# Optimization experiments

Hardware: AMD Instinct MI355X
Metric: run time of the kernel (lower is better)

The kernel has to match this reference:

```python
import jax, jax.numpy as jnp
import numpy as np

INC, ICS = 32, 8      # in_caps, in_caps_size
ONC, OCS = 32, 16     # out_caps, out_caps_size
K, STRIDE, PAD = 3, 1, 0
ITERS = 3


def squash(t, axis=-1):
    sq = jnp.sum(t * t, axis=axis, keepdims=True)
    return (sq / (1.0 + sq)) * t / jnp.sqrt(sq)


def setup_inputs() -> dict:
    key = jax.random.key(0)
    k1, k2 = jax.random.split(key)
    x = jax.random.normal(k1, (4, INC * ICS, 14, 14), dtype=jnp.float32)
    # nn.Parameter(torch.randn(...)); scaled by 1/sqrt(ICS) for numerical sanity
    weight = jax.random.normal(k2, (ONC, INC * K * K, ICS, OCS), dtype=jnp.float32) * (1.0 / np.sqrt(ICS))
    return {"x": x, "weight": weight}


def reference(x, weight):
    B, C, H, W = x.shape
    OH = (H + 2 * PAD - K) // STRIDE + 1
    OW = (W + 2 * PAD - K) // STRIDE + 1
    # Tile2d: extract KxK patches -> (B, C*K*K, OH, OW), channel order (C, kh, kw)
    patches = jax.lax.conv_general_dilated_patches(
        x, (K, K), (STRIDE, STRIDE), padding=((PAD, PAD), (PAD, PAD)))
    # (B, INC, ICS, K*K, OH*OW) -> (B, OH*OW, K*K, INC, ICS) -> (N, KK*INC, ICS)
    tiles = patches.reshape(B, INC, ICS, K * K, OH * OW)
    tiles = tiles.transpose(0, 4, 3, 1, 2).reshape(B * OH * OW, K * K * INC, ICS)

    # priors: (ONC, N, KKI, OCS)  == x[None,:,:,None,:] @ W[:,None]
    priors = jnp.einsum('nki,okic->onkc', tiles, weight)

    # dynamic routing; logits broadcast over OCS in the original (identical math)
    N = B * OH * OW
    KKI = K * K * INC
    logits = jnp.zeros((ONC, N, KKI, 1), dtype=priors.dtype)
    outputs = None
    for i in range(ITERS):
        probs = jax.nn.softmax(logits, axis=2)              # over KKI routes
        outputs = squash(jnp.sum(probs * priors, axis=2, keepdims=True))  # (ONC,N,1,OCS)
        if i != ITERS - 1:
            logits = logits + jnp.sum(priors * outputs, axis=-1, keepdims=True)

    # (ONC, N, OCS) -> (N, ONC, OCS) -> (B, ONC*OCS, OH, OW)
    out = outputs[:, :, 0, :].transpose(1, 0, 2)
    out = out.reshape(B, OH, OW, ONC * OCS).transpose(0, 3, 1, 2)
    return out
```

## Files before the change

kernel.cpp:

```cpp
#include <hip/hip_runtime.h>

static constexpr int OHW = 12, NSP = 144;

__global__ void build_T(const float* __restrict__ x, float4* __restrict__ T4) {
    const int g = blockIdx.x * 256 + threadIdx.x;
    const int n = g / 576;
    const int q = g - n * 576;
    const int r = q << 2;
    const int k = r >> 3;
    const int i0 = r & 7;
    const int ic = k & 31;
    const int kk = k >> 5;
    const int kh = kk / 3, kw = kk - kh * 3;
    const int b = n / NSP;
    const int rm = n - b * NSP;
    const int oh = rm / OHW, ow = rm - oh * OHW;
    const float* xp = x + (size_t)(b * 256 + ic * 8 + i0) * 196
                        + (oh + kh) * 14 + (ow + kw);
    float4 v;
    v.x = xp[0];
    v.y = xp[196];
    v.z = xp[392];
    v.w = xp[588];
    T4[g] = v;
}

__device__ __forceinline__ void fma4(float4& a, float s, const float4& w) {
    a.x = fmaf(s, w.x, a.x);
    a.y = fmaf(s, w.y, a.y);
    a.z = fmaf(s, w.z, a.z);
    a.w = fmaf(s, w.w, a.w);
}

__device__ __forceinline__ float4 shfl_xor4(const float4& v, int m) {
    float4 r;
    r.x = __shfl_xor(v.x, m);
    r.y = __shfl_xor(v.y, m);
    r.z = __shfl_xor(v.z, m);
    r.w = __shfl_xor(v.w, m);
    return r;
}

__device__ __forceinline__ void do_j(const float4* __restrict__ T4,
                                     const float4* __restrict__ W4,
                                     float4* __restrict__ Pl,
                                     int o, int nbase, int k, int cg,
                                     int g_local, int lane) {
    float4 w[8];
    const float4* wp = W4 + (size_t)(o * 288 + k) * 32 + cg;
    #pragma unroll
    for (int i = 0; i < 8; ++i) w[i] = wp[i * 4];
    #pragma unroll
    for (int nn = 0; nn < 4; ++nn) {
        const float4* tp = T4 + (size_t)(nbase + nn) * 576 + k * 2;
        const float4 t0 = tp[0];
        const float4 t1 = tp[1];
        float4 a = make_float4(0.f, 0.f, 0.f, 0.f);
        fma4(a, t0.x, w[0]); fma4(a, t0.y, w[1]);
        fma4(a, t0.z, w[2]); fma4(a, t0.w, w[3]);
        fma4(a, t1.x, w[4]); fma4(a, t1.y, w[5]);
        fma4(a, t1.z, w[6]); fma4(a, t1.w, w[7]);
        Pl[nn * 576 + g_local * 64 + lane] = a;
    }
}

__global__ __launch_bounds__(256, 4)
void caps_main(const float4* __restrict__ T4, const float4* __restrict__ W4,
               float* __restrict__ out) {
    __shared__ float4 Pl[4 * 9 * 64];
    const int tid = threadIdx.x;
    const int o = blockIdx.y;
    const int nbase = blockIdx.x * 4;
    const int cg = tid & 3;
    const int kg = tid >> 2;
    const int wv = tid >> 6;
    const int lane = tid & 63;

    float4 P[18];

    #pragma unroll
    for (int j = 0; j < 5; ++j) {
        const int k = kg + 64 * j;
        const int g = wv + 4 * j;
        if (k < 288 && g < 9)
            do_j(T4, W4, Pl, o, nbase, k, cg, g, lane);
    }
    __syncthreads();
    #pragma unroll
    for (int jj = 0; jj < 9; ++jj)
        P[jj] = Pl[wv * 576 + jj * 64 + lane];
    __syncthreads();
    #pragma unroll
    for (int j = 0; j < 5; ++j) {
        const int k = kg + 64 * j;
        const int g = wv + 4 * j;
        if (k < 288 && g >= 9)
            do_j(T4, W4, Pl, o, nbase, k, cg, g - 9, lane);
    }
    __syncthreads();
    #pragma unroll
    for (int jj = 9; jj < 18; ++jj)
        P[jj] = Pl[wv * 576 + (jj - 9) * 64 + lane];

    float lj[18];
    #pragma unroll
    for (int jj = 0; jj < 18; ++jj) lj[jj] = 0.f;
    float4 vq = make_float4(0.f, 0.f, 0.f, 0.f);

    #pragma unroll
    for (int it = 0; it < 3; ++it) {
        float4 svU = make_float4(0.f, 0.f, 0.f, 0.f);
        float S;
        if (it == 0) {
            #pragma unroll
            for (int jj = 0; jj < 18; ++jj) {
                svU.x += P[jj].x; svU.y += P[jj].y;
                svU.z += P[jj].z; svU.w += P[jj].w;
            }
            #pragma unroll
            for (int m = 4; m < 64; m <<= 1) {
                const float4 t = shfl_xor4(svU, m);
                svU.x += t.x; svU.y += t.y; svU.z += t.z; svU.w += t.w;
            }
            S = 288.0f;
        } else {
            S = 0.f;
            #pragma unroll
            for (int jj = 0; jj < 18; ++jj) {
                const float e = __expf(lj[jj]);
                S += e;
                fma4(svU, e, P[jj]);
            }
            #pragma unroll
            for (int m = 4; m < 64; m <<= 1) {
                const float4 t = shfl_xor4(svU, m);
                svU.x += t.x; svU.y += t.y; svU.z += t.z; svU.w += t.w;
                S += __shfl_xor(S, m);
            }
        }
        const float invS = __frcp_rn(S);
        float4 s;
        s.x = svU.x * invS; s.y = svU.y * invS;
        s.z = svU.z * invS; s.w = svU.w * invS;
        float sq = s.x * s.x + s.y * s.y + s.z * s.z + s.w * s.w;
        sq += __shfl_xor(sq, 1);
        sq += __shfl_xor(sq, 2);
        const float scale = __fsqrt_rn(sq) / (1.0f + sq);
        vq.x = s.x * scale; vq.y = s.y * scale;
        vq.z = s.z * scale; vq.w = s.w * scale;

        if (it < 2) {
            #pragma unroll
            for (int jj = 0; jj < 18; ++jj) {
                float d = P[jj].x * vq.x + P[jj].y * vq.y +
                          P[jj].z * vq.z + P[jj].w * vq.w;
                d += __shfl_xor(d, 1);
                d += __shfl_xor(d, 2);
                lj[jj] += d;
            }
        }
    }

    if ((lane >> 2) == 0) {
        const int n = nbase + wv;
        const int b = n / NSP;
        const int rm = n - b * NSP;
        float* op = out + (size_t)(b * 512 + o * 16 + cg * 4) * NSP + rm;
        op[0 * NSP] = vq.x;
        op[1 * NSP] = vq.y;
        op[2 * NSP] = vq.z;
        op[3 * NSP] = vq.w;
    }
}

extern "C" void kernel_launch(void* const* d_in, const int* in_sizes, int n_in,
                              void* d_out, int out_size, void* d_ws, size_t ws_size,
                              hipStream_t stream) {
    const float* x  = (const float*)d_in[0];
    const float* wt = (const float*)d_in[1];
    float* out = (float*)d_out;
    float4* T4 = (float4*)d_ws;

    build_T<<<dim3(576 * 576 / 256), 256, 0, stream>>>(x, T4);
    caps_main<<<dim3(144, 32), 256, 0, stream>>>(T4, (const float4*)wt, out);
}
```

Baseline: 125.4 us.

## Fuse patch extraction into capsule kernel using shared-memory input tiles

Removes the separate im2col kernel and its global workspace. Each block now loads a 3x8 spatial window of all 256 input channels into LDS with a swizzled layout, builds priors for 6 output positions directly from LDS, and routes them. The block grows to 384 threads (6 positions) in a 96x32 grid. This saves one launch and the T4 write/read traffic, at the cost of more LDS per block and occupancy changes.

Result: slower. 154.9 us (+23.5%).

```diff
diff --git a/kernel.cpp b/kernel.cpp
--- a/kernel.cpp
+++ b/kernel.cpp
@@ -1,29 +1,6 @@
 #include <hip/hip_runtime.h>
 
-static constexpr int OHW = 12, NSP = 144;
-
-__global__ void build_T(const float* __restrict__ x, float4* __restrict__ T4) {
-    const int g = blockIdx.x * 256 + threadIdx.x;
-    const int n = g / 576;
-    const int q = g - n * 576;
-    const int r = q << 2;
-    const int k = r >> 3;
-    const int i0 = r & 7;
-    const int ic = k & 31;
-    const int kk = k >> 5;
-    const int kh = kk / 3, kw = kk - kh * 3;
-    const int b = n / NSP;
-    const int rm = n - b * NSP;
-    const int oh = rm / OHW, ow = rm - oh * OHW;
-    const float* xp = x + (size_t)(b * 256 + ic * 8 + i0) * 196
-                        + (oh + kh) * 14 + (ow + kw);
-    float4 v;
-    v.x = xp[0];
-    v.y = xp[196];
-    v.z = xp[392];
-    v.w = xp[588];
-    T4[g] = v;
-}
+static constexpr int NSP = 144;
 
 __device__ __forceinline__ void fma4(float4& a, float s, const float4& w) {
     a.x = fmaf(s, w.x, a.x);
@@ -41,66 +18,75 @@
     return r;
 }
 
-__device__ __forceinline__ void do_j(const float4* __restrict__ T4,
-                                     const float4* __restrict__ W4,
-                                     float4* __restrict__ Pl,
-                                     int o, int nbase, int k, int cg,
-                                     int g_local, int lane) {
-    float4 w[8];
-    const float4* wp = W4 + (size_t)(o * 288 + k) * 32 + cg;
-    #pragma unroll
-    for (int i = 0; i < 8; ++i) w[i] = wp[i * 4];
-    #pragma unroll
-    for (int nn = 0; nn < 4; ++nn) {
-        const float4* tp = T4 + (size_t)(nbase + nn) * 576 + k * 2;
-        const float4 t0 = tp[0];
-        const float4 t1 = tp[1];
-        float4 a = make_float4(0.f, 0.f, 0.f, 0.f);
-        fma4(a, t0.x, w[0]); fma4(a, t0.y, w[1]);
-        fma4(a, t0.z, w[2]); fma4(a, t0.w, w[3]);
-        fma4(a, t1.x, w[4]); fma4(a, t1.y, w[5]);
-        fma4(a, t1.z, w[6]); fma4(a, t1.w, w[7]);
-        Pl[nn * 576 + g_local * 64 + lane] = a;
-    }
-}
+__global__ __launch_bounds__(384, 3)
+void caps_fused(const float* __restrict__ x, const float4* __restrict__ W4,
+                float* __restrict__ out) {
+    __shared__ float  Xl[24 * 32 * 12];
+    __shared__ float4 Pl[6 * 6 * 64];
 
-__global__ __launch_bounds__(256, 4)
-void caps_main(const float4* __restrict__ T4, const float4* __restrict__ W4,
-               float* __restrict__ out) {
-    __shared__ float4 Pl[4 * 9 * 64];
     const int tid = threadIdx.x;
-    const int o = blockIdx.y;
-    const int nbase = blockIdx.x * 4;
-    const int cg = tid & 3;
-    const int kg = tid >> 2;
-    const int wv = tid >> 6;
+    const int o   = blockIdx.y;
+    const int bx  = blockIdx.x;
+    const int b   = bx / 24;
+    const int r24 = bx - b * 24;
+    const int oh  = r24 >> 1;
+    const int ow0 = (r24 & 1) * 6;
+
+    const int cg   = tid & 3;
+    const int kg   = tid >> 2;
+    const int wv   = tid >> 6;
     const int lane = tid & 63;
 
+    {
+        const float* xb = x + (size_t)b * (256 * 196) + oh * 14 + ow0;
+        #pragma unroll
+        for (int it = 0; it < 16; ++it) {
+            const int e  = it * 384 + tid;
+            const int ch = e / 24;
+            const int sp = e - ch * 24;
+            const int r  = sp >> 3, c = sp & 7;
+            const int ic = ch >> 3, i = ch & 7;
+            const int icS = (ic + sp) & 31;
+            Xl[(sp * 32 + icS) * 12 + i] = xb[ch * 196 + r * 14 + c];
+        }
+    }
+    __syncthreads();
+
+    const float4* X4 = (const float4*)Xl;
     float4 P[18];
 
     #pragma unroll
-    for (int j = 0; j < 5; ++j) {
-        const int k = kg + 64 * j;
-        const int g = wv + 4 * j;
-        if (k < 288 && g < 9)
-            do_j(T4, W4, Pl, o, nbase, k, cg, g, lane);
+    for (int cch = 0; cch < 3; ++cch) {
+        const int k  = kg + 96 * cch;
+        const int ic = k & 31;
+        const int kk = k >> 5;
+        const int kh = kk / 3, kw = kk - kh * 3;
+
+        float4 w[8];
+        const float4* wp = W4 + ((size_t)(o * 288 + k) * 8) * 4 + cg;
+        #pragma unroll
+        for (int i = 0; i < 8; ++i) w[i] = wp[i * 4];
+
+        #pragma unroll
+        for (int nn = 0; nn < 6; ++nn) {
+            const int sp  = kh * 8 + nn + kw;
+            const int icS = (ic + sp) & 31;
+            const int b4  = (sp * 32 + icS) * 3;
+            const float4 t0 = X4[b4];
+            const float4 t1 = X4[b4 + 1];
+            float4 a = make_float4(0.f, 0.f, 0.f, 0.f);
+            fma4(a, t0.x, w[0]); fma4(a, t0.y, w[1]);
+            fma4(a, t0.z, w[2]); fma4(a, t0.w, w[3]);
+            fma4(a, t1.x, w[4]); fma4(a, t1.y, w[5]);
+            fma4(a, t1.z, w[6]); fma4(a, t1.w, w[7]);
+            Pl[nn * 384 + wv * 64 + lane] = a;
+        }
+        __syncthreads();
+        #pragma unroll
+        for (int jjl = 0; jjl < 6; ++jjl)
+            P[cch * 6 + jjl] = Pl[wv * 384 + jjl * 64 + lane];
+        if (cch < 2) __syncthreads();
     }
-    __syncthreads();
-    #pragma unroll
-    for (int jj = 0; jj < 9; ++jj)
-        P[jj] = Pl[wv * 576 + jj * 64 + lane];
-    __syncthreads();
-    #pragma unroll
-    for (int j = 0; j < 5; ++j) {
-        const int k = kg + 64 * j;
-        const int g = wv + 4 * j;
-        if (k < 288 && g >= 9)
-            do_j(T4, W4, Pl, o, nbase, k, cg, g - 9, lane);
-    }
-    __syncthreads();
-    #pragma unroll
-    for (int jj = 9; jj < 18; ++jj)
-        P[jj] = Pl[wv * 576 + (jj - 9) * 64 + lane];
 
     float lj[18];
     #pragma unroll
@@ -162,9 +148,7 @@
     }
 
     if ((lane >> 2) == 0) {
-        const int n = nbase + wv;
-        const int b = n / NSP;
-        const int rm = n - b * NSP;
+        const int rm = oh * 12 + ow0 + wv;
         float* op = out + (size_t)(b * 512 + o * 16 + cg * 4) * NSP + rm;
         op[0 * NSP] = vq.x;
         op[1 * NSP] = vq.y;
@@ -179,8 +163,7 @@
     const float* x  = (const float*)d_in[0];
     const float* wt = (const float*)d_in[1];
     float* out = (float*)d_out;
-    float4* T4 = (float4*)d_ws;
+    (void)d_ws; (void)ws_size;
 
-    build_T<<<dim3(576 * 576 / 256), 256, 0, stream>>>(x, T4);
-    caps_main<<<dim3(144, 32), 256, 0, stream>>>(T4, (const float4*)wt, out);
+    caps_fused<<<dim3(96, 32), 384, 0, stream>>>(x, (const float4*)wt, out);
 }
```

## Split each spatial position's routing across two waves with 512-thread blocks

Applied to the files above, without the earlier changes.

Doubles the block size to 512 threads so each spatial position's 288 routes are split across two wavefronts, each holding 9 priors in registers instead of 18. The prior production is restructured into three passes over shared memory, and the routing reductions are combined across the wave pair through small shared buffers with a barrier on each iteration. The intent is to cut register pressure and raise occupancy and parallelism. The cost is extra block-wide synchronisation and shared-memory exchange in every routing iteration.

Result: slower. 184.5 us (+47.1%).

```diff
diff --git a/kernel.cpp b/kernel.cpp
--- a/kernel.cpp
+++ b/kernel.cpp
@@ -41,103 +41,108 @@
     return r;
 }
 
-__device__ __forceinline__ void do_j(const float4* __restrict__ T4,
-                                     const float4* __restrict__ W4,
-                                     float4* __restrict__ Pl,
-                                     int o, int nbase, int k, int cg,
-                                     int g_local, int lane) {
-    float4 w[8];
-    const float4* wp = W4 + (size_t)(o * 288 + k) * 32 + cg;
-    #pragma unroll
-    for (int i = 0; i < 8; ++i) w[i] = wp[i * 4];
-    #pragma unroll
-    for (int nn = 0; nn < 4; ++nn) {
-        const float4* tp = T4 + (size_t)(nbase + nn) * 576 + k * 2;
-        const float4 t0 = tp[0];
-        const float4 t1 = tp[1];
-        float4 a = make_float4(0.f, 0.f, 0.f, 0.f);
-        fma4(a, t0.x, w[0]); fma4(a, t0.y, w[1]);
-        fma4(a, t0.z, w[2]); fma4(a, t0.w, w[3]);
-        fma4(a, t1.x, w[4]); fma4(a, t1.y, w[5]);
-        fma4(a, t1.z, w[6]); fma4(a, t1.w, w[7]);
-        Pl[nn * 576 + g_local * 64 + lane] = a;
-    }
-}
-
-__global__ __launch_bounds__(256, 4)
+__global__ __launch_bounds__(512, 6)
 void caps_main(const float4* __restrict__ T4, const float4* __restrict__ W4,
                float* __restrict__ out) {
-    __shared__ float4 Pl[4 * 9 * 64];
-    const int tid = threadIdx.x;
-    const int o = blockIdx.y;
+    __shared__ float4 Pl[4 * 8 * 64];
+    __shared__ float4 ExV[3][4][2][4];
+    __shared__ float  ExS[2][4][2];
+
+    const int tid  = threadIdx.x;
+    const int o    = blockIdx.y;
     const int nbase = blockIdx.x * 4;
-    const int cg = tid & 3;
-    const int kg = tid >> 2;
-    const int wv = tid >> 6;
+    const int cg   = tid & 3;
+    const int kg   = tid >> 2;
+    const int wv   = tid >> 6;
     const int lane = tid & 63;
+    const int nn   = wv >> 1;
+    const int h    = wv & 1;
 
-    float4 P[18];
+    float4 P[9];
 
-    #pragma unroll
-    for (int j = 0; j < 5; ++j) {
-        const int k = kg + 64 * j;
-        const int g = wv + 4 * j;
-        if (k < 288 && g < 9)
-            do_j(T4, W4, Pl, o, nbase, k, cg, g, lane);
+    auto produce = [&](int k) {
+        float4 w[8];
+        const float4* wp = W4 + (size_t)(o * 288 + k) * 32 + cg;
+        #pragma unroll
+        for (int i = 0; i < 8; ++i) w[i] = wp[i * 4];
+        #pragma unroll
+        for (int m = 0; m < 4; ++m) {
+            const float4* tp = T4 + (size_t)(nbase + m) * 576 + k * 2;
+            const float4 t0 = tp[0];
+            const float4 t1 = tp[1];
+            float4 a = make_float4(0.f, 0.f, 0.f, 0.f);
+            fma4(a, t0.x, w[0]); fma4(a, t0.y, w[1]);
+            fma4(a, t0.z, w[2]); fma4(a, t0.w, w[3]);
+            fma4(a, t1.x, w[4]); fma4(a, t1.y, w[5]);
+            fma4(a, t1.z, w[6]); fma4(a, t1.w, w[7]);
+            Pl[m * 512 + wv * 64 + lane] = a;
+        }
+    };
+
+    const float4* Pn = &Pl[nn * 512];
+
+    produce(kg);
+    __syncthreads();
+    if (h == 0) {
+        #pragma unroll
+        for (int s = 0; s < 8; ++s) P[s] = Pn[s * 64 + lane];
     }
     __syncthreads();
-    #pragma unroll
-    for (int jj = 0; jj < 9; ++jj)
-        P[jj] = Pl[wv * 576 + jj * 64 + lane];
+
+    produce(kg + 128);
     __syncthreads();
-    #pragma unroll
-    for (int j = 0; j < 5; ++j) {
-        const int k = kg + 64 * j;
-        const int g = wv + 4 * j;
-        if (k < 288 && g >= 9)
-            do_j(T4, W4, Pl, o, nbase, k, cg, g - 9, lane);
+    if (h == 0) {
+        P[8] = Pn[lane];
+    } else {
+        #pragma unroll
+        for (int s = 1; s < 8; ++s) P[s - 1] = Pn[s * 64 + lane];
     }
     __syncthreads();
+
+    if (kg < 32) produce(kg + 256);
+    __syncthreads();
+    if (h == 1) {
+        P[7] = Pn[lane];
+        P[8] = Pn[64 + lane];
+    }
+
+    float lj[9];
     #pragma unroll
-    for (int jj = 9; jj < 18; ++jj)
-        P[jj] = Pl[wv * 576 + (jj - 9) * 64 + lane];
-
-    float lj[18];
-    #pragma unroll
-    for (int jj = 0; jj < 18; ++jj) lj[jj] = 0.f;
+    for (int pl = 0; pl < 9; ++pl) lj[pl] = 0.f;
     float4 vq = make_float4(0.f, 0.f, 0.f, 0.f);
 
     #pragma unroll
     for (int it = 0; it < 3; ++it) {
         float4 svU = make_float4(0.f, 0.f, 0.f, 0.f);
-        float S;
+        float Sp = 0.f;
         if (it == 0) {
             #pragma unroll
-            for (int jj = 0; jj < 18; ++jj) {
-                svU.x += P[jj].x; svU.y += P[jj].y;
-                svU.z += P[jj].z; svU.w += P[jj].w;
+            for (int pl = 0; pl < 9; ++pl) {
+                svU.x += P[pl].x; svU.y += P[pl].y;
+                svU.z += P[pl].z; svU.w += P[pl].w;
             }
+        } else {
             #pragma unroll
-            for (int m = 4; m < 64; m <<= 1) {
-                const float4 t = shfl_xor4(svU, m);
-                svU.x += t.x; svU.y += t.y; svU.z += t.z; svU.w += t.w;
-            }
-            S = 288.0f;
-        } else {
-            S = 0.f;
-            #pragma unroll
-            for (int jj = 0; jj < 18; ++jj) {
-                const float e = __expf(lj[jj]);
-                S += e;
-                fma4(svU, e, P[jj]);
-            }
-            #pragma unroll
-            for (int m = 4; m < 64; m <<= 1) {
-                const float4 t = shfl_xor4(svU, m);
-                svU.x += t.x; svU.y += t.y; svU.z += t.z; svU.w += t.w;
-                S += __shfl_xor(S, m);
+            for (int pl = 0; pl < 9; ++pl) {
+                const float e = __expf(lj[pl]);
+                Sp += e;
+                fma4(svU, e, P[pl]);
             }
         }
+        #pragma unroll
+        for (int m = 4; m < 64; m <<= 1) {
+            const float4 t = shfl_xor4(svU, m);
+            svU.x += t.x; svU.y += t.y; svU.z += t.z; svU.w += t.w;
+            if (it != 0) Sp += __shfl_xor(Sp, m);
+        }
+        if ((lane >> 2) == 0) {
+            ExV[it][nn][h][cg] = svU;
+            if (it != 0 && lane == 0) ExS[it - 1][nn][h] = Sp;
+        }
+        __syncthreads();
+        const float4 t = ExV[it][nn][h ^ 1][cg];
+        svU.x += t.x; svU.y += t.y; svU.z += t.z; svU.w += t.w;
+        const float S = (it == 0) ? 288.0f : (Sp + ExS[it - 1][nn][h ^ 1]);
         const float invS = __frcp_rn(S);
         float4 s;
         s.x = svU.x * invS; s.y = svU.y * invS;
@@ -151,18 +156,18 @@
 
         if (it < 2) {
             #pragma unroll
-            for (int jj = 0; jj < 18; ++jj) {
-                float d = P[jj].x * vq.x + P[jj].y * vq.y +
-                          P[jj].z * vq.z + P[jj].w * vq.w;
+            for (int pl = 0; pl < 9; ++pl) {
+                float d = P[pl].x * vq.x + P[pl].y * vq.y +
+                          P[pl].z * vq.z + P[pl].w * vq.w;
                 d += __shfl_xor(d, 1);
                 d += __shfl_xor(d, 2);
-                lj[jj] += d;
+                lj[pl] += d;
             }
         }
     }
 
-    if ((lane >> 2) == 0) {
-        const int n = nbase + wv;
+    if (h == 0 && (lane >> 2) == 0) {
+        const int n = nbase + nn;
         const int b = n / NSP;
         const int rm = n - b * NSP;
         float* op = out + (size_t)(b * 512 + o * 16 + cg * 4) * NSP + rm;
@@ -182,5 +187,5 @@
     float4* T4 = (float4*)d_ws;
 
     build_T<<<dim3(576 * 576 / 256), 256, 0, stream>>>(x, T4);
-    caps_main<<<dim3(144, 32), 256, 0, stream>>>(T4, (const float4*)wt, out);
+    caps_main<<<dim3(144, 32), 512, 0, stream>>>(T4, (const float4*)wt, out);
 }
```

## Double spatial positions per block to reuse loaded weights across eight positions

Applied to the files above, without the earlier changes.

Blocks grow to 512 threads and each handles 8 spatial positions instead of 4. Each thread's 8 loaded weight float4s are now reused across 8 positions, which halves weight traffic per prior computed. The route-to-lane mapping is simplified into three produce passes of 128/128/32 routes staged through a 64KB shared buffer. The cost is higher LDS use per block, which limits resident blocks per CU, and a grid of half as many blocks.

New measurement: 126.6 us. No clear change (+1.0%).

```diff
diff --git a/kernel.cpp b/kernel.cpp
--- a/kernel.cpp
+++ b/kernel.cpp
@@ -41,66 +41,58 @@
     return r;
 }
 
-__device__ __forceinline__ void do_j(const float4* __restrict__ T4,
-                                     const float4* __restrict__ W4,
-                                     float4* __restrict__ Pl,
-                                     int o, int nbase, int k, int cg,
-                                     int g_local, int lane) {
-    float4 w[8];
-    const float4* wp = W4 + (size_t)(o * 288 + k) * 32 + cg;
-    #pragma unroll
-    for (int i = 0; i < 8; ++i) w[i] = wp[i * 4];
-    #pragma unroll
-    for (int nn = 0; nn < 4; ++nn) {
-        const float4* tp = T4 + (size_t)(nbase + nn) * 576 + k * 2;
-        const float4 t0 = tp[0];
-        const float4 t1 = tp[1];
-        float4 a = make_float4(0.f, 0.f, 0.f, 0.f);
-        fma4(a, t0.x, w[0]); fma4(a, t0.y, w[1]);
-        fma4(a, t0.z, w[2]); fma4(a, t0.w, w[3]);
-        fma4(a, t1.x, w[4]); fma4(a, t1.y, w[5]);
-        fma4(a, t1.z, w[6]); fma4(a, t1.w, w[7]);
-        Pl[nn * 576 + g_local * 64 + lane] = a;
-    }
-}
-
-__global__ __launch_bounds__(256, 4)
+__global__ __launch_bounds__(512, 3)
 void caps_main(const float4* __restrict__ T4, const float4* __restrict__ W4,
                float* __restrict__ out) {
-    __shared__ float4 Pl[4 * 9 * 64];
-    const int tid = threadIdx.x;
-    const int o = blockIdx.y;
-    const int nbase = blockIdx.x * 4;
-    const int cg = tid & 3;
-    const int kg = tid >> 2;
-    const int wv = tid >> 6;
-    const int lane = tid & 63;
+    __shared__ float4 Pl[8 * 8 * 64];
+
+    const int tid   = threadIdx.x;
+    const int o     = blockIdx.y;
+    const int nbase = blockIdx.x * 8;
+    const int cg    = tid & 3;
+    const int kg    = tid >> 2;
+    const int wv    = tid >> 6;
+    const int lane  = tid & 63;
 
     float4 P[18];
 
-    #pragma unroll
-    for (int j = 0; j < 5; ++j) {
-        const int k = kg + 64 * j;
-        const int g = wv + 4 * j;
-        if (k < 288 && g < 9)
-            do_j(T4, W4, Pl, o, nbase, k, cg, g, lane);
-    }
+    auto produce = [&](int k) {
+        float4 w[8];
+        const float4* wp = W4 + (size_t)(o * 288 + k) * 32 + cg;
+        #pragma unroll
+        for (int i = 0; i < 8; ++i) w[i] = wp[i * 4];
+        #pragma unroll
+        for (int m = 0; m < 8; ++m) {
+            const float4* tp = T4 + (size_t)(nbase + m) * 576 + k * 2;
+            const float4 t0 = tp[0];
+            const float4 t1 = tp[1];
+            float4 a = make_float4(0.f, 0.f, 0.f, 0.f);
+            fma4(a, t0.x, w[0]); fma4(a, t0.y, w[1]);
+            fma4(a, t0.z, w[2]); fma4(a, t0.w, w[3]);
+            fma4(a, t1.x, w[4]); fma4(a, t1.y, w[5]);
+            fma4(a, t1.z, w[6]); fma4(a, t1.w, w[7]);
+            Pl[m * 512 + wv * 64 + lane] = a;
+        }
+    };
+
+    const float4* Pn = &Pl[wv * 512];
+
+    produce(kg);
     __syncthreads();
     #pragma unroll
-    for (int jj = 0; jj < 9; ++jj)
-        P[jj] = Pl[wv * 576 + jj * 64 + lane];
+    for (int s = 0; s < 8; ++s) P[s] = Pn[s * 64 + lane];
+    __syncthreads();
+
+    produce(kg + 128);
     __syncthreads();
     #pragma unroll
-    for (int j = 0; j < 5; ++j) {
-        const int k = kg + 64 * j;
-        const int g = wv + 4 * j;
-        if (k < 288 && g >= 9)
-            do_j(T4, W4, Pl, o, nbase, k, cg, g - 9, lane);
-    }
+    for (int s = 0; s < 8; ++s) P[8 + s] = Pn[s * 64 + lane];
     __syncthreads();
-    #pragma unroll
-    for (int jj = 9; jj < 18; ++jj)
-        P[jj] = Pl[wv * 576 + (jj - 9) * 64 + lane];
+
+    if (kg < 32) produce(kg + 256);
+    __syncthreads();
+    P[16] = Pn[lane];
+    P[17] = Pn[64 + lane];
 
     float lj[18];
     #pragma unroll
@@ -182,5 +174,5 @@
     float4* T4 = (float4*)d_ws;
 
     build_T<<<dim3(576 * 576 / 256), 256, 0, stream>>>(x, T4);
-    caps_main<<<dim3(144, 32), 256, 0, stream>>>(T4, (const float4*)wt, out);
+    caps_main<<<dim3(72, 32), 512, 0, stream>>>(T4, (const float4*)wt, out);
 }
```
